# Kernel tuning notes

Hardware: AMD Instinct MI355X
Metric: run time of the kernel (lower is better)

Reference implementation:

```python
import jax, jax.numpy as jnp
import numpy as np

N = 16384; C = 16; H = 256; W = 704
HEADS = 4; PTS = 4; K = 8; DH = C // HEADS
EPS = 1e-3  # BatchNorm eps from module

def _bn(x, g, b):
    # BatchNorm1d in training mode: batch statistics over N
    mu = x.mean(axis=0)
    var = x.var(axis=0)
    return (x - mu) * jax.lax.rsqrt(var + EPS) * g + b

def setup_inputs():
    key = jax.random.key(0)
    ks = jax.random.split(key, 20)
    def w(i, shape, s=0.25):
        return jax.random.normal(ks[i], shape, jnp.float32) * s
    grid_y = jax.random.randint(ks[0], (N,), 0, H)
    grid_x = jax.random.randint(ks[1], (N,), 0, W)
    return {
        "point_features": jax.random.normal(ks[2], (N, C), jnp.float32),
        "image_feat": jax.random.normal(ks[3], (C, H, W), jnp.float32),
        "image_grid": jnp.stack([grid_y, grid_x], axis=1),
        "Wk": w(4, (C, C)), "bk": w(5, (C,)), "gk": jnp.ones((C,)), "betak": jnp.zeros((C,)),
        "Wfc": w(6, (2, C)), "bfc": w(7, (C,)), "gfc": jnp.ones((C,)), "betafc": jnp.zeros((C,)),
        "Wt": w(8, (C, C)), "bt": w(9, (C,)), "gt": jnp.ones((C,)), "betat": jnp.zeros((C,)),
        "Woff": w(10, (C, HEADS * PTS * 2), 0.02), "boff": w(11, (HEADS * PTS * 2,), 0.5),
        "Wattn": w(12, (C, HEADS * PTS), 0.02), "battn": jnp.zeros((HEADS * PTS,)),
        "Wval": w(13, (C, C)), "bval": w(14, (C,)),
        "Wout": w(15, (C, C)), "bout": w(16, (C,)),
        "Wf": w(17, (2 * C, C)), "bf": w(18, (C,)), "gf": jnp.ones((C,)), "betaf": jnp.zeros((C,)),
    }

def _deform_attn(q, image_feat, grid_f, Woff, boff, Wattn, battn, Wval, bval, Wout, bout):
    # MSDeformAttn with 1 level: learned offsets around projected pixel, bilinear sampling
    n = q.shape[0]
    off = (q @ Woff + boff).reshape(n, HEADS, PTS, 2)
    attn = jax.nn.softmax((q @ Wattn + battn).reshape(n, HEADS, PTS), axis=-1)
    val = (image_feat.reshape(C, H * W).T @ Wval + bval).reshape(H * W, HEADS, DH)
    val_h = val.transpose(1, 0, 2)  # [HEADS, HW, DH]
    loc_y = grid_f[:, 0][:, None, None] + off[..., 0]  # [N, HEADS, PTS]
    loc_x = grid_f[:, 1][:, None, None] + off[..., 1]
    y0 = jnp.floor(loc_y); x0 = jnp.floor(loc_x)
    wy = loc_y - y0; wx = loc_x - x0

    def corner(yi, xi, wgt):
        valid = (yi >= 0) & (yi <= H - 1) & (xi >= 0) & (xi <= W - 1)
        yc = jnp.clip(yi, 0, H - 1).astype(jnp.int32)
        xc = jnp.clip(xi, 0, W - 1).astype(jnp.int32)
        idx = (yc * W + xc).transpose(1, 0, 2)  # [HEADS, N, PTS]
        g = jax.vmap(lambda v, i: v[i])(val_h, idx)  # [HEADS, N, PTS, DH]
        return g * (wgt * valid).transpose(1, 0, 2)[..., None]

    samp = (corner(y0, x0, (1 - wy) * (1 - wx))
            + corner(y0, x0 + 1, (1 - wy) * wx)
            + corner(y0 + 1, x0, wy * (1 - wx))
            + corner(y0 + 1, x0 + 1, wy * wx))  # [HEADS, N, PTS, DH]
    out = (samp * attn.transpose(1, 0, 2)[..., None]).sum(axis=2)  # [HEADS, N, DH]
    out = out.transpose(1, 0, 2).reshape(n, C)
    return out @ Wout + bout

def reference(point_features, image_feat, image_grid, Wk, bk, gk, betak, Wfc, bfc, gfc, betafc, Wt, bt, gt, betat, Woff, boff, Wattn, battn, Wval, bval, Wout, bout, Wf, bf, gf, betaf):
    grid_f = image_grid.astype(jnp.float32)
    # KNN over projected pixel coords (cKDTree.query k=K+1, drop self)
    d2 = ((grid_f[:, None, :] - grid_f[None, :, :]) ** 2).sum(-1)
    _, nidx = jax.lax.top_k(-d2, K + 1)
    nidx = nidx[:, 1:]  # [N, K]

    pts = _bn(point_features @ Wk + bk, gk, betak)  # pts_key_proj
    # normalized relative image-plane positions -> fc
    center = grid_f.mean(axis=0)
    rel = grid_f - center
    mx = jnp.abs(rel).max(axis=0)
    mx = jnp.where(mx == 0, 1.0, mx)
    pos = _bn((rel / mx) @ Wfc + bfc, gfc, betafc)

    # gather image feats at projected pixels + KNN-graph neighbor aggregation
    gathered = image_feat[:, image_grid[:, 0], image_grid[:, 1]].T  # [N, C]
    neigh = gathered[nidx].mean(axis=1)  # [N, C]

    q = pts + pos
    img_pre = _deform_attn(q, image_feat, grid_f, Woff, boff, Wattn, battn, Wval, bval, Wout, bout) + neigh

    pts_pre = _bn(pts @ Wt + bt, gt, betat)  # pts_transform
    fuse = jax.nn.relu(jnp.concatenate([pts_pre, img_pre], axis=-1))  # activate_out
    return jax.nn.relu(_bn(fuse @ Wf + bf, gf, betaf))  # fuse_conv
```

## Files before the change

### kernel.cpp

```cpp
#include <hip/hip_runtime.h>
#include <climits>

#define N_ 16384
#define C_ 16
#define H_ 256
#define W_ 704
#define HW_ (H_*W_)
#define NC_ (N_*C_)
#define EPS_ 1e-3f
#define HDR_ 512

typedef unsigned long long ull;


#define VAL_  (HDR_ + 9*NC_)
#define KNNI_ (VAL_ + HW_*16)
#define PARTF_ (KNNI_ + 378256)

__device__ __forceinline__ float wsum64(float v){
#pragma unroll
  for (int o = 32; o > 0; o >>= 1) v += __shfl_down(v, o);
  return v;
}

#define LOAD16(dst, src) { const float4* _s=(const float4*)(src); float4 _a=_s[0],_b=_s[1],_c=_s[2],_d=_s[3]; \
  dst[0]=_a.x;dst[1]=_a.y;dst[2]=_a.z;dst[3]=_a.w; dst[4]=_b.x;dst[5]=_b.y;dst[6]=_b.z;dst[7]=_b.w; \
  dst[8]=_c.x;dst[9]=_c.y;dst[10]=_c.z;dst[11]=_c.w; dst[12]=_d.x;dst[13]=_d.y;dst[14]=_d.z;dst[15]=_d.w; }

#define STORE16(dst, src) { float4* _d=(float4*)(dst); \
  _d[0]=make_float4(src[0],src[1],src[2],src[3]); _d[1]=make_float4(src[4],src[5],src[6],src[7]); \
  _d[2]=make_float4(src[8],src[9],src[10],src[11]); _d[3]=make_float4(src[12],src[13],src[14],src[15]); }

__global__ __launch_bounds__(256) void k_init(float* ws){
  if (blockIdx.x < 176){
    int4* c = (int4*)(ws + KNNI_);
    c[blockIdx.x*256 + threadIdx.x] = make_int4(0,0,0,0);
  } else if (threadIdx.x == 0){
    int* ih = (int*)ws;
    ih[0]=0; ih[1]=0; ih[2]=INT_MAX; ih[3]=INT_MIN; ih[4]=INT_MAX; ih[5]=INT_MIN;
  }
}

__global__ __launch_bounds__(256) void k_gridcnt(const int* __restrict__ grid, float* __restrict__ ws){
  int i = blockIdx.x*256 + threadIdx.x;
  int2 p = ((const int2*)grid)[i];
  int* counts = (int*)(ws + KNNI_);
  atomicAdd(&counts[p.x*W_ + p.y], 1);
  int sy=p.x, sx=p.y, mny=p.x, mxy=p.x, mnx=p.y, mxx=p.y;
#pragma unroll
  for (int o=32;o>0;o>>=1){
    sy += __shfl_down(sy,o); sx += __shfl_down(sx,o);
    mny = min(mny,__shfl_down(mny,o)); mxy = max(mxy,__shfl_down(mxy,o));
    mnx = min(mnx,__shfl_down(mnx,o)); mxx = max(mxx,__shfl_down(mxx,o));
  }
  __shared__ int sh[24];
  int w = threadIdx.x >> 6;
  if ((threadIdx.x & 63) == 0){
    sh[w]=sy; sh[4+w]=sx; sh[8+w]=mny; sh[12+w]=mxy; sh[16+w]=mnx; sh[20+w]=mxx;
  }
  __syncthreads();
  if (threadIdx.x == 0){
    int a0=sh[0]+sh[1]+sh[2]+sh[3];
    int a1=sh[4]+sh[5]+sh[6]+sh[7];
    int a2=min(min(sh[8],sh[9]),min(sh[10],sh[11]));
    int a3=max(max(sh[12],sh[13]),max(sh[14],sh[15]));
    int a4=min(min(sh[16],sh[17]),min(sh[18],sh[19]));
    int a5=max(max(sh[20],sh[21]),max(sh[22],sh[23]));
    int* ih = (int*)ws;
    atomicAdd(&ih[0],a0); atomicAdd(&ih[1],a1);
    atomicMin(&ih[2],a2); atomicMax(&ih[3],a3);
    atomicMin(&ih[4],a4); atomicMax(&ih[5],a5);
  }
}

__global__ __launch_bounds__(256) void k_scanA(float* ws){
  const int* counts = (const int*)(ws + KNNI_);
  int* bsum = (int*)(ws + KNNI_) + 180224 + 180240;
  int t = threadIdx.x;
  int v = counts[blockIdx.x*256 + t];
#pragma unroll
  for (int o=32;o>0;o>>=1) v += __shfl_down(v,o);
  __shared__ int w4[4];
  if ((t&63)==0) w4[t>>6] = v;
  __syncthreads();
  if (t==0) bsum[blockIdx.x] = w4[0]+w4[1]+w4[2]+w4[3];
}

__global__ __launch_bounds__(256) void k_scanB(float* ws){
  if (threadIdx.x == 0){
    int* ih = (int*)ws;
    float cy = (float)ih[0] / (float)N_;
    float cx = (float)ih[1] / (float)N_;
    float my = fmaxf((float)ih[3]-cy, cy-(float)ih[2]);
    float mx = fmaxf((float)ih[5]-cx, cx-(float)ih[4]);
    if (my == 0.f) my = 1.f;
    if (mx == 0.f) mx = 1.f;
    ws[264]=cy; ws[265]=cx; ws[266]=1.f/my; ws[267]=1.f/mx;
  }
  int* bsum = (int*)(ws + KNNI_) + 180224 + 180240;
  int* boff = bsum + 704;
  __shared__ int tmp[256];
  __shared__ int carry;
  int t = threadIdx.x;
  if (t==0) carry = 0;
  __syncthreads();
  for (int c=0;c<3;++c){
    int idx = c*256 + t;
    int v = (idx < 704) ? bsum[idx] : 0;
    tmp[t] = v;
    __syncthreads();
    for (int o=1;o<256;o<<=1){
      int x = (t>=o) ? tmp[t-o] : 0;
      __syncthreads();
      tmp[t] += x;
      __syncthreads();
    }
    int incl = tmp[t];
    int base = carry;
    if (idx < 704) boff[idx] = base + incl - v;
    __syncthreads();
    if (t==255) carry = base + incl;
    __syncthreads();
  }
}

__global__ __launch_bounds__(256) void k_scanC(float* ws){
  int* counts = (int*)(ws + KNNI_);
  int* cellst = counts + 180224;
  const int* boff = counts + 180224 + 180240 + 704;
  __shared__ int tmp[256];
  int t = threadIdx.x;
  int i = blockIdx.x*256 + t;
  int v = counts[i];
  tmp[t] = v;
  __syncthreads();
  for (int o=1;o<256;o<<=1){
    int x = (t>=o) ? tmp[t-o] : 0;
    __syncthreads();
    tmp[t] += x;
    __syncthreads();
  }
  int start = boff[blockIdx.x] + tmp[t] - v;
  cellst[i] = start;
  counts[i] = start;
  if (i == 0) cellst[HW_] = N_;
}

__global__ __launch_bounds__(256) void k_scatter(const int* __restrict__ grid, float* __restrict__ ws){
  int i = blockIdx.x*256 + threadIdx.x;
  int2 g = ((const int2*)grid)[i];
  int* counts = (int*)(ws + KNNI_);
  unsigned* psort = (unsigned*)(counts + 180224 + 180240 + 704 + 704);
  int pos = atomicAdd(&counts[g.x*W_ + g.y], 1);
  psort[pos] = ((unsigned)g.x<<24) | ((unsigned)g.y<<14) | (unsigned)i;
}

__global__ __launch_bounds__(256) void k_gath(const float* __restrict__ imf,
                                              const int* __restrict__ grid,
                                              float* __restrict__ ws){
  int idx = blockIdx.x*256 + threadIdx.x;
  int i = idx >> 4, c = idx & 15;
  int2 g = ((const int2*)grid)[i];
  ws[HDR_ + 2*NC_ + idx] = imf[c*HW_ + g.x*W_ + g.y];
}

__global__ __launch_bounds__(64) void k_knn2(float* __restrict__ ws){
  int gid = blockIdx.x*64 + threadIdx.x;
  const int* cellst = (const int*)(ws + KNNI_) + 180224;
  const unsigned* psort = (const unsigned*)((const int*)(ws + KNNI_) + 180224 + 180240 + 704 + 704);
  unsigned me = psort[gid];
  int y = (int)(me>>24), x = (int)((me>>14)&1023), i = (int)(me&16383);
  int r = 8;
  for (;;){
    int y0=max(y-r,0), y1=min(y+r,H_-1), x0=max(x-r,0), x1=min(x+r,W_-1);
    bool covered = (y0==0)&&(y1==H_-1)&&(x0==0)&&(x1==W_-1);
    int area = (y1-y0+1)*(x1-x0+1);
    if (area >= 224 || covered) break;
    r += 8;
  }
  ull arr[9];
  for (;;){
    int y0=max(y-r,0), y1=min(y+r,H_-1), x0=max(x-r,0), x1=min(x+r,W_-1);
    bool covered = (y0==0)&&(y1==H_-1)&&(x0==0)&&(x1==W_-1);
#pragma unroll
    for (int q=0;q<9;++q) arr[q] = ~0ull;
    for (int yy=y0; yy<=y1; ++yy){
      int rowb = yy*W_;
      int s = cellst[rowb + x0];
      int e = cellst[rowb + x1 + 1];
      for (int p=s; p<e; ++p){
        unsigned u = psort[p];
        int py = (int)(u>>24), px = (int)((u>>14)&1023), pi = (int)(u&16383);
        int dy = y-py, dx = x-px;
        int d2 = dy*dy + dx*dx;
        ull key = ((ull)(unsigned)d2 << 14) | (unsigned)pi;
        if (key < arr[8]){
          int q = 8;
          while (q > 0 && arr[q-1] > key){ arr[q] = arr[q-1]; --q; }
          arr[q] = key;
        }
      }
    }
    if (covered) break;
    if (arr[8] != ~0ull){
      int d9 = (int)(arr[8] >> 14);
      if (d9 < (r+1)*(r+1)) break;
    }
    r <<= 1;
  }
  const float* gath = ws + HDR_ + 2*NC_;
  float acc[16];
#pragma unroll
  for (int c=0;c<16;++c) acc[c] = 0.f;
  for (int nb=1; nb<9; ++nb){
    int idx = (int)(arr[nb] & 16383ull);
    const float4* s4 = (const float4*)(gath + idx*16);
#pragma unroll
    for (int rq=0; rq<4; ++rq){
      float4 v = s4[rq];
      acc[rq*4]+=v.x; acc[rq*4+1]+=v.y; acc[rq*4+2]+=v.z; acc[rq*4+3]+=v.w;
    }
  }
  float* neigh = ws + HDR_ + 7*NC_;
  float o[16];
#pragma unroll
  for (int c=0;c<16;++c) o[c] = acc[c]*0.125f;
  STORE16(neigh + i*16, o);
}

__global__ __launch_bounds__(64) void k_lin1(
    const float* __restrict__ pf, const int* __restrict__ grid,
    const float* __restrict__ Wk, const float* __restrict__ bk,
    const float* __restrict__ Wfc, const float* __restrict__ bfc,
    float* __restrict__ ws)
{
  __shared__ float sWk[256], sbk[16], sWfc[32], sbfc[16];
  int t = threadIdx.x;
  for (int j=t;j<256;j+=64) sWk[j] = Wk[j];
  if (t < 16){ sbk[t]=bk[t]; sbfc[t]=bfc[t]; }
  if (t < 32) sWfc[t] = Wfc[t];
  __syncthreads();
  int i = blockIdx.x*64 + t;
  float p[16]; LOAD16(p, pf + i*16);
  float ok[16];
#pragma unroll
  for (int c=0;c<16;++c) ok[c] = sbk[c];
#pragma unroll
  for (int j=0;j<16;++j){ float v = p[j];
#pragma unroll
    for (int c=0;c<16;++c) ok[c] += v*sWk[j*16+c];
  }
  float* pts_lin = ws + HDR_;
  STORE16(pts_lin + i*16, ok);
  float cy=ws[264], cx=ws[265], imy=ws[266], imx=ws[267];
  int2 g = ((const int2*)grid)[i];
  float ry = ((float)g.x - cy)*imy, rx = ((float)g.y - cx)*imx;
  float op[16];
#pragma unroll
  for (int c=0;c<16;++c) op[c] = ry*sWfc[c] + rx*sWfc[16+c] + sbfc[c];
  float* pos_lin = ws + HDR_ + NC_;
  STORE16(pos_lin + i*16, op);
  float* partK  = ws + VAL_;
  float* partFC = ws + VAL_ + 8192;
#pragma unroll
  for (int c=0;c<16;++c){
    float a = wsum64(ok[c]); float b = wsum64(ok[c]*ok[c]);
    if (t==0){ partK[blockIdx.x*32+c]=a; partK[blockIdx.x*32+16+c]=b; }
    a = wsum64(op[c]); b = wsum64(op[c]*op[c]);
    if (t==0){ partFC[blockIdx.x*32+c]=a; partFC[blockIdx.x*32+16+c]=b; }
  }
}

__device__ __forceinline__ void red1_body(const float* __restrict__ g, const float* __restrict__ b,
                                          float* __restrict__ ws, int partOff, int aOff, float* red){
  int t = threadIdx.x, slot = t & 31, chunk = t >> 5;
  const float* part = ws + partOff;
  float acc = 0.f;
  for (int bb=chunk*32; bb<chunk*32+32; ++bb) acc += part[bb*32 + slot];
  red[t] = acc;
  __syncthreads();
  if (chunk == 0){
    float v = red[slot];
#pragma unroll
    for (int k2=1;k2<8;++k2) v += red[k2*32+slot];
    red[slot] = v;
  }
  __syncthreads();
  if (t < 16){
    float mu  = red[t]    * (1.f/N_);
    float var = red[16+t] * (1.f/N_) - mu*mu;
    float a = g[t] / sqrtf(var + EPS_);
    ws[aOff+t]    = a;
    ws[aOff+16+t] = b[t] - mu*a;
  }
  __syncthreads();
}

__global__ __launch_bounds__(256) void k_red2(const float* __restrict__ gk, const float* __restrict__ betak,
                                              const float* __restrict__ gfc, const float* __restrict__ betafc,
                                              float* __restrict__ ws){
  __shared__ float red[256];
  red1_body(gk, betak, ws, VAL_, 136, red);
  red1_body(gfc, betafc, ws, VAL_+8192, 168, red);
}

__global__ __launch_bounds__(256) void k_red1(const float* __restrict__ g, const float* __restrict__ b,
                                              float* __restrict__ ws, int partOff, int aOff){
  __shared__ float red[256];
  red1_body(g, b, ws, partOff, aOff, red);
}

__global__ __launch_bounds__(64) void k_qstage(
    const float* __restrict__ Wt, const float* __restrict__ bt,
    const float* __restrict__ Woff, const float* __restrict__ boff,
    const float* __restrict__ Wattn, const float* __restrict__ battn,
    float* __restrict__ ws)
{
  __shared__ float sWt[256], sWoff[512], sWattn[256];
  __shared__ float sbt[16], sboff[32], sbattn[16];
  __shared__ float skA[16], skC[16], sfcA[16], sfcC[16];
  int t = threadIdx.x;
  for (int j=t;j<256;j+=64){ sWt[j]=Wt[j]; sWattn[j]=Wattn[j]; }
  for (int j=t;j<512;j+=64) sWoff[j]=Woff[j];
  if (t<16){ sbt[t]=bt[t]; sbattn[t]=battn[t];
    skA[t]=ws[136+t]; skC[t]=ws[152+t]; sfcA[t]=ws[168+t]; sfcC[t]=ws[184+t]; }
  if (t<32) sboff[t]=boff[t];
  __syncthreads();
  int i = blockIdx.x*64 + t;
  float* pts_lin = ws + HDR_;
  float* pos_lin = ws + HDR_ + NC_;
  float* t_lin   = ws + HDR_ + 3*NC_;
  float* offp    = ws + HDR_ + 4*NC_;
  float* attnp   = ws + HDR_ + 6*NC_;
  float pl[16], po[16];
  LOAD16(pl, pts_lin + i*16);
  LOAD16(po, pos_lin + i*16);
  float pts[16], q[16];
#pragma unroll
  for (int c=0;c<16;++c){ pts[c] = pl[c]*skA[c]+skC[c]; q[c] = pts[c] + po[c]*sfcA[c]+sfcC[c]; }
  float tv[16];
#pragma unroll
  for (int c=0;c<16;++c) tv[c] = sbt[c];
#pragma unroll
  for (int j=0;j<16;++j){ float v=pts[j];
#pragma unroll
    for (int c=0;c<16;++c) tv[c] += v*sWt[j*16+c];
  }
  STORE16(t_lin + i*16, tv);
  float* partT = ws + VAL_ + 16384;
#pragma unroll
  for (int c=0;c<16;++c){
    float a = wsum64(tv[c]); float b = wsum64(tv[c]*tv[c]);
    if (t==0){ partT[blockIdx.x*32+c]=a; partT[blockIdx.x*32+16+c]=b; }
  }
  float ov[32];
#pragma unroll
  for (int o=0;o<32;++o) ov[o] = sboff[o];
#pragma unroll
  for (int j=0;j<16;++j){ float v=q[j];
#pragma unroll
    for (int o=0;o<32;++o) ov[o] += v*sWoff[j*32+o];
  }
  { float4* d=(float4*)(offp + i*32);
#pragma unroll
    for (int r=0;r<8;++r) d[r]=make_float4(ov[r*4],ov[r*4+1],ov[r*4+2],ov[r*4+3]);
  }
  float l[16];
#pragma unroll
  for (int c=0;c<16;++c) l[c] = sbattn[c];
#pragma unroll
  for (int j=0;j<16;++j){ float v=q[j];
#pragma unroll
    for (int c=0;c<16;++c) l[c] += v*sWattn[j*16+c];
  }
  float av[16];
#pragma unroll
  for (int h=0;h<4;++h){
    float m = fmaxf(fmaxf(l[h*4],l[h*4+1]),fmaxf(l[h*4+2],l[h*4+3]));
    float e0=expf(l[h*4]-m), e1=expf(l[h*4+1]-m), e2=expf(l[h*4+2]-m), e3=expf(l[h*4+3]-m);
    float inv = 1.f/(e0+e1+e2+e3);
    av[h*4]=e0*inv; av[h*4+1]=e1*inv; av[h*4+2]=e2*inv; av[h*4+3]=e3*inv;
  }
  STORE16(attnp + i*16, av);
}

__global__ __launch_bounds__(256) void k_val(const float* __restrict__ imf,
    const float* __restrict__ Wval, const float* __restrict__ bval, float* __restrict__ ws)
{
  __shared__ float sW[256], sb[16];
  int t = threadIdx.x;
  sW[t] = Wval[t];
  if (t < 16) sb[t] = bval[t];
  __syncthreads();
  int pix = blockIdx.x*256 + t;
  float a[16];
#pragma unroll
  for (int ci=0;ci<16;++ci) a[ci] = imf[ci*HW_ + pix];
  float o[16];
#pragma unroll
  for (int c=0;c<16;++c) o[c] = sb[c];
#pragma unroll
  for (int ci=0;ci<16;++ci){ float v=a[ci];
#pragma unroll
    for (int c=0;c<16;++c) o[c] += v*sW[ci*16+c];
  }
  float* val = ws + VAL_;
  STORE16(val + pix*16, o);
}

__global__ __launch_bounds__(256) void k_attn(
    const int* __restrict__ grid,
    const float* __restrict__ Wout, const float* __restrict__ bout,
    const float* __restrict__ Wf, const float* __restrict__ bf,
    float* __restrict__ ws)
{
  __shared__ float sWout[256], sWf[512], sbout[16], sbf[16];
  __shared__ float sTl[1024], sNei[1024], sSamp[1024], sImg[1024];
  __shared__ float sPart[128];
  int t = threadIdx.x;
  int p = t >> 2, h = t & 3;
  int i = blockIdx.x*64 + p;
  sWout[t]=Wout[t]; sWf[t]=Wf[t]; sWf[t+256]=Wf[t+256];
  if (t<16){ sbout[t]=bout[t]; sbf[t]=bf[t]; }
  {
    const float4* tl4 = (const float4*)(ws + HDR_ + 3*NC_ + blockIdx.x*1024);
    const float4* nv4 = (const float4*)(ws + HDR_ + 7*NC_ + blockIdx.x*1024);
    float4 v = tl4[t];
    int c0 = (t*4) & 15;
    float a0=ws[200+c0],a1=ws[200+c0+1],a2=ws[200+c0+2],a3=ws[200+c0+3];
    float c0v=ws[216+c0],c1v=ws[216+c0+1],c2v=ws[216+c0+2],c3v=ws[216+c0+3];
    sTl[t*4]   = fmaxf(v.x*a0+c0v, 0.f);
    sTl[t*4+1] = fmaxf(v.y*a1+c1v, 0.f);
    sTl[t*4+2] = fmaxf(v.z*a2+c2v, 0.f);
    sTl[t*4+3] = fmaxf(v.w*a3+c3v, 0.f);
    float4 nv = nv4[t];
    sNei[t*4]=nv.x; sNei[t*4+1]=nv.y; sNei[t*4+2]=nv.z; sNei[t*4+3]=nv.w;
  }
  const float4* off4 = (const float4*)(ws + HDR_ + 4*NC_ + blockIdx.x*2048);
  float4 o0 = off4[t*2], o1 = off4[t*2+1];
  float4 aw = ((const float4*)(ws + HDR_ + 6*NC_ + blockIdx.x*1024))[t];
  int2 g = ((const int2*)grid)[i];
  float y = (float)g.x, x = (float)g.y;
  const float4* val4 = (const float4*)(ws + VAL_);
  float4 acc = make_float4(0.f,0.f,0.f,0.f);
  float offv[8] = {o0.x,o0.y,o0.z,o0.w,o1.x,o1.y,o1.z,o1.w};
  float avv[4]  = {aw.x,aw.y,aw.z,aw.w};
#define CORNER(yy,xx,wgt) do{ int _y=(yy),_x=(xx); \
    if ((unsigned)_y < (unsigned)H_ && (unsigned)_x < (unsigned)W_){ \
      float4 _v = val4[(_y*W_+_x)*4 + h]; float _w = a*(wgt); \
      acc.x += _w*_v.x; acc.y += _w*_v.y; acc.z += _w*_v.z; acc.w += _w*_v.w; } }while(0)
#pragma unroll
  for (int pt=0; pt<4; ++pt){
    float a  = avv[pt];
    float ly = y + offv[pt*2], lx = x + offv[pt*2+1];
    float fy = floorf(ly), fx = floorf(lx);
    float wy = ly - fy, wx = lx - fx;
    int y0 = (int)fy, x0 = (int)fx;
    CORNER(y0,   x0,   (1.f-wy)*(1.f-wx));
    CORNER(y0,   x0+1, (1.f-wy)*wx);
    CORNER(y0+1, x0,   wy*(1.f-wx));
    CORNER(y0+1, x0+1, wy*wx);
  }
#undef CORNER
  ((float4*)sSamp)[t] = acc;
  __syncthreads();
  float img[4];
#pragma unroll
  for (int k=0;k<4;++k){ int cc=h*4+k; img[k] = sbout[cc] + sNei[p*16+cc]; }
#pragma unroll
  for (int j=0;j<16;++j){
    float v = sSamp[p*16+j];
#pragma unroll
    for (int k=0;k<4;++k) img[k] += v*sWout[j*16 + h*4 + k];
  }
  ((float4*)sImg)[t] = make_float4(img[0],img[1],img[2],img[3]);
  __syncthreads();
  float fl[4];
#pragma unroll
  for (int k=0;k<4;++k) fl[k] = sbf[h*4+k];
#pragma unroll
  for (int j=0;j<16;++j){
    float v1 = sTl[p*16+j];
    float v2 = fmaxf(sImg[p*16+j], 0.f);
#pragma unroll
    for (int k=0;k<4;++k){
      fl[k] += v1*sWf[j*16 + h*4 + k];
      fl[k] += v2*sWf[(16+j)*16 + h*4 + k];
    }
  }
  float* f_lin = ws + HDR_ + 8*NC_;
  ((float4*)(f_lin + blockIdx.x*1024))[t] = make_float4(fl[0],fl[1],fl[2],fl[3]);
  float s0=fl[0],s1=fl[1],s2=fl[2],s3=fl[3];
  float q0=fl[0]*fl[0],q1=fl[1]*fl[1],q2=fl[2]*fl[2],q3=fl[3]*fl[3];
#pragma unroll
  for (int o=32;o>=4;o>>=1){
    s0+=__shfl_down(s0,o); s1+=__shfl_down(s1,o); s2+=__shfl_down(s2,o); s3+=__shfl_down(s3,o);
    q0+=__shfl_down(q0,o); q1+=__shfl_down(q1,o); q2+=__shfl_down(q2,o); q3+=__shfl_down(q3,o);
  }
  int wave = t >> 6, lane = t & 63;
  if (lane < 4){
    sPart[wave*32 + lane*4+0]=s0; sPart[wave*32 + lane*4+1]=s1;
    sPart[wave*32 + lane*4+2]=s2; sPart[wave*32 + lane*4+3]=s3;
    sPart[wave*32 + 16 + lane*4+0]=q0; sPart[wave*32 + 16 + lane*4+1]=q1;
    sPart[wave*32 + 16 + lane*4+2]=q2; sPart[wave*32 + 16 + lane*4+3]=q3;
  }
  __syncthreads();
  if (t < 32){
    float v = sPart[t]+sPart[32+t]+sPart[64+t]+sPart[96+t];
    (ws + PARTF_)[blockIdx.x*32 + t] = v;
  }
}

__global__ __launch_bounds__(256) void k_out(const float* __restrict__ ws, float* __restrict__ out){
  int idx = blockIdx.x*256 + threadIdx.x;
  int c = idx & 15;
  float v = ws[HDR_ + 8*NC_ + idx];
  out[idx] = fmaxf(v*ws[232+c] + ws[248+c], 0.f);
}

extern "C" void kernel_launch(void* const* d_in, const int* in_sizes, int n_in,
                              void* d_out, int out_size, void* d_ws, size_t ws_size,
                              hipStream_t stream)
{
  const float* pf    = (const float*)d_in[0];
  const float* imf   = (const float*)d_in[1];
  const int*   gridp = (const int*)d_in[2];
  const float* Wk   =(const float*)d_in[3],  *bk   =(const float*)d_in[4];
  const float* gk   =(const float*)d_in[5],  *betak=(const float*)d_in[6];
  const float* Wfc  =(const float*)d_in[7],  *bfc  =(const float*)d_in[8];
  const float* gfc  =(const float*)d_in[9],  *betafc=(const float*)d_in[10];
  const float* Wt   =(const float*)d_in[11], *bt   =(const float*)d_in[12];
  const float* gt   =(const float*)d_in[13], *betat=(const float*)d_in[14];
  const float* Woff =(const float*)d_in[15], *boff =(const float*)d_in[16];
  const float* Wattn=(const float*)d_in[17], *battn=(const float*)d_in[18];
  const float* Wval =(const float*)d_in[19], *bval =(const float*)d_in[20];
  const float* Wout =(const float*)d_in[21], *bout =(const float*)d_in[22];
  const float* Wf   =(const float*)d_in[23], *bf   =(const float*)d_in[24];
  const float* gf   =(const float*)d_in[25], *betaf=(const float*)d_in[26];
  float* ws  = (float*)d_ws;
  float* out = (float*)d_out;

  hipLaunchKernelGGL(k_init,     dim3(177),     dim3(256), 0, stream, ws);
  hipLaunchKernelGGL(k_gridcnt,  dim3(N_/256),  dim3(256), 0, stream, gridp, ws);
  hipLaunchKernelGGL(k_scanA,    dim3(704),     dim3(256), 0, stream, ws);
  hipLaunchKernelGGL(k_scanB,    dim3(1),       dim3(256), 0, stream, ws);
  hipLaunchKernelGGL(k_scanC,    dim3(704),     dim3(256), 0, stream, ws);
  hipLaunchKernelGGL(k_scatter,  dim3(N_/256),  dim3(256), 0, stream, gridp, ws);
  hipLaunchKernelGGL(k_gath,     dim3(NC_/256), dim3(256), 0, stream, imf, gridp, ws);
  hipLaunchKernelGGL(k_lin1,     dim3(N_/64),   dim3(64),  0, stream, pf, gridp, Wk, bk, Wfc, bfc, ws);
  hipLaunchKernelGGL(k_red2,     dim3(1),       dim3(256), 0, stream, gk, betak, gfc, betafc, ws);
  hipLaunchKernelGGL(k_qstage,   dim3(N_/64),   dim3(64),  0, stream, Wt, bt, Woff, boff, Wattn, battn, ws);
  hipLaunchKernelGGL(k_red1,     dim3(1),       dim3(256), 0, stream, gt, betat, ws, VAL_+16384, 200);
  hipLaunchKernelGGL(k_val,      dim3(HW_/256), dim3(256), 0, stream, imf, Wval, bval, ws);
  hipLaunchKernelGGL(k_knn2,     dim3(N_/64),   dim3(64),  0, stream, ws);
  hipLaunchKernelGGL(k_attn,     dim3(N_/64),   dim3(256), 0, stream, gridp, Wout, bout, Wf, bf, ws);
  hipLaunchKernelGGL(k_red1,     dim3(1),       dim3(256), 0, stream, gf, betaf, ws, PARTF_, 232);
  hipLaunchKernelGGL(k_out,      dim3(NC_/256), dim3(256), 0, stream, ws, out);
}
```

Baseline: 275.0 us.

## Parallelize KNN across 4 lanes per point with LDS band cache, fuse gather/val kernels

The KNN kernel now uses four lanes per query point. Each lane scans every fourth row of the search window, and the lanes merge their partial top-9 lists with shuffles. The block first caches the sorted points of its row band in shared memory and binary-searches each row for the x range, falling back to global memory when the band is too large. The gather and value-projection kernels are merged into one launch, and the scan kernels switch from an LDS Hillis-Steele scan to wave shuffle scans. Partial-stat buffers move to new workspace offsets so they no longer alias the value buffer. The costs are extra merge logic, more divergence during expansion rounds, and 24KB of LDS per block.

```diff
diff --git a/kernel.cpp b/kernel.cpp
--- a/kernel.cpp
+++ b/kernel.cpp
@@ -13,9 +13,14 @@
 typedef unsigned long long ull;
 
 
-#define VAL_  (HDR_ + 9*NC_)
-#define KNNI_ (VAL_ + HW_*16)
+#define VAL_   (HDR_ + 9*NC_)
+#define KNNI_  (VAL_ + HW_*16)
 #define PARTF_ (KNNI_ + 378256)
+#define PK_    (PARTF_ + 8192)
+#define PFC_   (PARTF_ + 16384)
+#define PT_    (PARTF_ + 24576)
+
+#define CAP_ 6144
 
 __device__ __forceinline__ float wsum64(float v){
 #pragma unroll
@@ -99,27 +104,24 @@
   }
   int* bsum = (int*)(ws + KNNI_) + 180224 + 180240;
   int* boff = bsum + 704;
-  __shared__ int tmp[256];
-  __shared__ int carry;
-  int t = threadIdx.x;
-  if (t==0) carry = 0;
+  __shared__ int sWsum[4];
+  __shared__ int sCarry;
+  int t = threadIdx.x, lane = t & 63, wv = t >> 6;
+  if (t==0) sCarry = 0;
   __syncthreads();
   for (int c=0;c<3;++c){
     int idx = c*256 + t;
-    int v = (idx < 704) ? bsum[idx] : 0;
-    tmp[t] = v;
+    int v0 = (idx < 704) ? bsum[idx] : 0;
+    int v = v0;
+#pragma unroll
+    for (int o=1;o<64;o<<=1){ int xx=__shfl_up(v,o); if (lane>=o) v+=xx; }
+    if (lane==63) sWsum[wv]=v;
     __syncthreads();
-    for (int o=1;o<256;o<<=1){
-      int x = (t>=o) ? tmp[t-o] : 0;
-      __syncthreads();
-      tmp[t] += x;
-      __syncthreads();
-    }
-    int incl = tmp[t];
-    int base = carry;
-    if (idx < 704) boff[idx] = base + incl - v;
+    int add = sCarry;
+    for (int w2=0;w2<wv;++w2) add += sWsum[w2];
+    if (idx < 704) boff[idx] = add + v - v0;
     __syncthreads();
-    if (t==255) carry = base + incl;
+    if (t==255) sCarry = add + v;
     __syncthreads();
   }
 }
@@ -128,19 +130,17 @@
   int* counts = (int*)(ws + KNNI_);
   int* cellst = counts + 180224;
   const int* boff = counts + 180224 + 180240 + 704;
-  __shared__ int tmp[256];
-  int t = threadIdx.x;
+  __shared__ int sWsum[4];
+  int t = threadIdx.x, lane = t & 63, wv = t >> 6;
   int i = blockIdx.x*256 + t;
-  int v = counts[i];
-  tmp[t] = v;
-  __syncthreads();
-  for (int o=1;o<256;o<<=1){
-    int x = (t>=o) ? tmp[t-o] : 0;
-    __syncthreads();
-    tmp[t] += x;
-    __syncthreads();
-  }
-  int start = boff[blockIdx.x] + tmp[t] - v;
+  int v0 = counts[i], v = v0;
+#pragma unroll
+  for (int o=1;o<64;o<<=1){ int xx=__shfl_up(v,o); if (lane>=o) v+=xx; }
+  if (lane==63) sWsum[wv]=v;
+  __syncthreads();
+  int add = boff[blockIdx.x];
+  for (int w2=0;w2<wv;++w2) add += sWsum[w2];
+  int start = add + v - v0;
   cellst[i] = start;
   counts[i] = start;
   if (i == 0) cellst[HW_] = N_;
@@ -155,77 +155,184 @@
   psort[pos] = ((unsigned)g.x<<24) | ((unsigned)g.y<<14) | (unsigned)i;
 }
 
-__global__ __launch_bounds__(256) void k_gath(const float* __restrict__ imf,
+__global__ __launch_bounds__(256) void k_prep(const float* __restrict__ imf,
                                               const int* __restrict__ grid,
+                                              const float* __restrict__ Wval,
+                                              const float* __restrict__ bval,
                                               float* __restrict__ ws){
-  int idx = blockIdx.x*256 + threadIdx.x;
-  int i = idx >> 4, c = idx & 15;
-  int2 g = ((const int2*)grid)[i];
-  ws[HDR_ + 2*NC_ + idx] = imf[c*HW_ + g.x*W_ + g.y];
-}
-
-__global__ __launch_bounds__(64) void k_knn2(float* __restrict__ ws){
-  int gid = blockIdx.x*64 + threadIdx.x;
+  int t = threadIdx.x;
+  if (blockIdx.x < 1024){
+    int idx = blockIdx.x*256 + t;
+    int i = idx >> 4, c = idx & 15;
+    int2 g = ((const int2*)grid)[i];
+    ws[HDR_ + 2*NC_ + idx] = imf[c*HW_ + g.x*W_ + g.y];
+  } else {
+    __shared__ float sW[256], sb[16];
+    sW[t] = Wval[t];
+    if (t < 16) sb[t] = bval[t];
+    __syncthreads();
+    int pix = (blockIdx.x-1024)*256 + t;
+    float a[16];
+#pragma unroll
+    for (int ci=0;ci<16;++ci) a[ci] = imf[ci*HW_ + pix];
+    float o[16];
+#pragma unroll
+    for (int c=0;c<16;++c) o[c] = sb[c];
+#pragma unroll
+    for (int ci=0;ci<16;++ci){ float v=a[ci];
+#pragma unroll
+      for (int c=0;c<16;++c) o[c] += v*sW[ci*16+c];
+    }
+    float* val = ws + VAL_;
+    STORE16(val + pix*16, o);
+  }
+}
+
+__device__ __forceinline__ void knn_insert(ull* arr, ull key){
+  if (key < arr[8]){
+    int q = 8;
+    while (q > 0 && arr[q-1] > key){ arr[q] = arr[q-1]; --q; }
+    arr[q] = key;
+  }
+}
+
+__device__ __forceinline__ void scan_rows_global(const int* __restrict__ cellst,
+                                                 const unsigned* __restrict__ psort,
+                                                 int y, int x, int s,
+                                                 int y0, int y1, int x0, int x1, ull* arr){
+  for (int yy=y0+s; yy<=y1; yy+=4){
+    int rowb = yy*W_;
+    int st = cellst[rowb + x0];
+    int e  = cellst[rowb + x1 + 1];
+    int dy = y-yy, dy2 = dy*dy;
+    for (int p=st; p<e; ++p){
+      unsigned u = psort[p];
+      int px = (int)((u>>14)&1023);
+      int dx = x-px;
+      knn_insert(arr, ((ull)(unsigned)(dy2+dx*dx) << 14) | (ull)(u & 16383u));
+    }
+  }
+}
+
+__global__ __launch_bounds__(256) void k_knn4(float* __restrict__ ws){
   const int* cellst = (const int*)(ws + KNNI_) + 180224;
   const unsigned* psort = (const unsigned*)((const int*)(ws + KNNI_) + 180224 + 180240 + 704 + 704);
+  __shared__ unsigned sBand[CAP_];
+  __shared__ int sRowBase[80];
+  __shared__ int sMn, sMx;
+  int tid = threadIdx.x, lane = tid & 63;
+  int s = tid & 3, pl = tid >> 2;
+  int gid = blockIdx.x*64 + pl;
   unsigned me = psort[gid];
   int y = (int)(me>>24), x = (int)((me>>14)&1023), i = (int)(me&16383);
+  if (tid==0){ sMn = INT_MAX; sMx = -1; }
+  __syncthreads();
+  if (s==0){ atomicMin(&sMn, y); atomicMax(&sMx, y); }
+  __syncthreads();
+  int ya = max(sMn-16,0), yb = min(sMx+16,H_-1);
+  int nr = yb-ya+1;
+  int p0 = cellst[ya*W_], p1 = cellst[(yb+1)*W_];
+  int count = p1-p0;
+  bool fb = (count > CAP_) || (nr > 78);
+  if (!fb){
+    for (int j=tid; j<count; j+=256) sBand[j] = psort[p0+j];
+    for (int j=tid; j<=nr; j+=256) sRowBase[j] = cellst[(ya+j)*W_] - p0;
+  }
+  __syncthreads();
   int r = 8;
-  for (;;){
-    int y0=max(y-r,0), y1=min(y+r,H_-1), x0=max(x-r,0), x1=min(x+r,W_-1);
-    bool covered = (y0==0)&&(y1==H_-1)&&(x0==0)&&(x1==W_-1);
-    int area = (y1-y0+1)*(x1-x0+1);
-    if (area >= 224 || covered) break;
-    r += 8;
-  }
+  { int y0=max(y-8,0),y1=min(y+8,H_-1),x0=max(x-8,0),x1=min(x+8,W_-1);
+    if ((y1-y0+1)*(x1-x0+1) < 224) r = 16; }
   ull arr[9];
-  for (;;){
-    int y0=max(y-r,0), y1=min(y+r,H_-1), x0=max(x-r,0), x1=min(x+r,W_-1);
-    bool covered = (y0==0)&&(y1==H_-1)&&(x0==0)&&(x1==W_-1);
-#pragma unroll
-    for (int q=0;q<9;++q) arr[q] = ~0ull;
-    for (int yy=y0; yy<=y1; ++yy){
-      int rowb = yy*W_;
-      int s = cellst[rowb + x0];
-      int e = cellst[rowb + x1 + 1];
-      for (int p=s; p<e; ++p){
-        unsigned u = psort[p];
-        int py = (int)(u>>24), px = (int)((u>>14)&1023), pi = (int)(u&16383);
-        int dy = y-py, dx = x-px;
-        int d2 = dy*dy + dx*dx;
-        ull key = ((ull)(unsigned)d2 << 14) | (unsigned)pi;
-        if (key < arr[8]){
-          int q = 8;
-          while (q > 0 && arr[q-1] > key){ arr[q] = arr[q-1]; --q; }
-          arr[q] = key;
+#pragma unroll
+  for (int q=0;q<9;++q) arr[q] = ~0ull;
+  {
+    int y0=max(y-r,0),y1=min(y+r,H_-1),x0=max(x-r,0),x1=min(x+r,W_-1);
+    if (!fb){
+      for (int yy=y0+s; yy<=y1; yy+=4){
+        int j = yy-ya;
+        int b = sRowBase[j], e = sRowBase[j+1];
+        int lo=b, hi=e;
+        while (lo<hi){ int mid=(lo+hi)>>1; int xm=(int)((sBand[mid]>>14)&1023); if (xm<x0) lo=mid+1; else hi=mid; }
+        int dy = y-yy, dy2 = dy*dy;
+        for (int p=lo; p<e; ++p){
+          unsigned u = sBand[p];
+          int px = (int)((u>>14)&1023);
+          if (px > x1) break;
+          int dx = x-px;
+          knn_insert(arr, ((ull)(unsigned)(dy2+dx*dx) << 14) | (ull)(u & 16383u));
         }
       }
-    }
-    if (covered) break;
-    if (arr[8] != ~0ull){
-      int d9 = (int)(arr[8] >> 14);
-      if (d9 < (r+1)*(r+1)) break;
-    }
-    r <<= 1;
+    } else {
+      scan_rows_global(cellst, psort, y, x, s, y0, y1, x0, x1, arr);
+    }
+  }
+  ull m[9];
+  bool done = false;
+  {
+    ull k[9];
+#pragma unroll
+    for (int q=0;q<9;++q) m[q] = ~0ull;
+    int base = lane & ~3;
+    for (int ss=0; ss<4; ++ss){
+#pragma unroll
+      for (int q=0;q<9;++q) k[q] = __shfl(arr[q], base+ss);
+      for (int q2=0;q2<9;++q2){
+        ull kk = k[q2];
+        if (kk >= m[8]) break;
+        int q = 8; while (q>0 && m[q-1]>kk){ m[q]=m[q-1]; --q; } m[q]=kk;
+      }
+    }
+    int y0=max(y-r,0),y1=min(y+r,H_-1),x0=max(x-r,0),x1=min(x+r,W_-1);
+    bool covered = (y0==0)&&(y1==H_-1)&&(x0==0)&&(x1==W_-1);
+    bool ok = covered;
+    if (!ok && m[8] != ~0ull){ int d9 = (int)(m[8]>>14); ok = d9 < (r+1)*(r+1); }
+    done = ok;
+  }
+  while (__ballot(!done)){
+    if (!done){
+      r <<= 1;
+      int y0=max(y-r,0),y1=min(y+r,H_-1),x0=max(x-r,0),x1=min(x+r,W_-1);
+#pragma unroll
+      for (int q=0;q<9;++q) arr[q] = ~0ull;
+      scan_rows_global(cellst, psort, y, x, s, y0, y1, x0, x1, arr);
+    }
+    ull k[9];
+    bool doIns = !done;
+    if (doIns){
+#pragma unroll
+      for (int q=0;q<9;++q) m[q] = ~0ull;
+    }
+    int base = lane & ~3;
+    for (int ss=0; ss<4; ++ss){
+#pragma unroll
+      for (int q=0;q<9;++q) k[q] = __shfl(arr[q], base+ss);
+      if (doIns){
+        for (int q2=0;q2<9;++q2){
+          ull kk = k[q2];
+          if (kk >= m[8]) break;
+          int q = 8; while (q>0 && m[q-1]>kk){ m[q]=m[q-1]; --q; } m[q]=kk;
+        }
+      }
+    }
+    if (!done){
+      int y0=max(y-r,0),y1=min(y+r,H_-1),x0=max(x-r,0),x1=min(x+r,W_-1);
+      bool covered = (y0==0)&&(y1==H_-1)&&(x0==0)&&(x1==W_-1);
+      bool ok = covered;
+      if (!ok && m[8] != ~0ull){ int d9 = (int)(m[8]>>14); ok = d9 < (r+1)*(r+1); }
+      if (ok) done = true;
+    }
   }
   const float* gath = ws + HDR_ + 2*NC_;
-  float acc[16];
-#pragma unroll
-  for (int c=0;c<16;++c) acc[c] = 0.f;
+  float4 acc = make_float4(0.f,0.f,0.f,0.f);
+#pragma unroll
   for (int nb=1; nb<9; ++nb){
-    int idx = (int)(arr[nb] & 16383ull);
-    const float4* s4 = (const float4*)(gath + idx*16);
-#pragma unroll
-    for (int rq=0; rq<4; ++rq){
-      float4 v = s4[rq];
-      acc[rq*4]+=v.x; acc[rq*4+1]+=v.y; acc[rq*4+2]+=v.z; acc[rq*4+3]+=v.w;
-    }
+    int idx = (int)(m[nb] & 16383ull);
+    const float4 g = *(const float4*)(gath + idx*16 + s*4);
+    acc.x += g.x; acc.y += g.y; acc.z += g.z; acc.w += g.w;
   }
   float* neigh = ws + HDR_ + 7*NC_;
-  float o[16];
-#pragma unroll
-  for (int c=0;c<16;++c) o[c] = acc[c]*0.125f;
-  STORE16(neigh + i*16, o);
+  *(float4*)(neigh + i*16 + s*4) =
+      make_float4(acc.x*0.125f, acc.y*0.125f, acc.z*0.125f, acc.w*0.125f);
 }
 
 __global__ __launch_bounds__(64) void k_lin1(
@@ -260,8 +367,8 @@
   for (int c=0;c<16;++c) op[c] = ry*sWfc[c] + rx*sWfc[16+c] + sbfc[c];
   float* pos_lin = ws + HDR_ + NC_;
   STORE16(pos_lin + i*16, op);
-  float* partK  = ws + VAL_;
-  float* partFC = ws + VAL_ + 8192;
+  float* partK  = ws + PK_;
+  float* partFC = ws + PFC_;
 #pragma unroll
   for (int c=0;c<16;++c){
     float a = wsum64(ok[c]); float b = wsum64(ok[c]*ok[c]);
@@ -300,8 +407,8 @@
                                               const float* __restrict__ gfc, const float* __restrict__ betafc,
                                               float* __restrict__ ws){
   __shared__ float red[256];
-  red1_body(gk, betak, ws, VAL_, 136, red);
-  red1_body(gfc, betafc, ws, VAL_+8192, 168, red);
+  red1_body(gk, betak, ws, PK_, 136, red);
+  red1_body(gfc, betafc, ws, PFC_, 168, red);
 }
 
 __global__ __launch_bounds__(256) void k_red1(const float* __restrict__ g, const float* __restrict__ b,
@@ -347,7 +454,7 @@
     for (int c=0;c<16;++c) tv[c] += v*sWt[j*16+c];
   }
   STORE16(t_lin + i*16, tv);
-  float* partT = ws + VAL_ + 16384;
+  float* partT = ws + PT_;
 #pragma unroll
   for (int c=0;c<16;++c){
     float a = wsum64(tv[c]); float b = wsum64(tv[c]*tv[c]);
@@ -382,30 +489,6 @@
     av[h*4]=e0*inv; av[h*4+1]=e1*inv; av[h*4+2]=e2*inv; av[h*4+3]=e3*inv;
   }
   STORE16(attnp + i*16, av);
-}
-
-__global__ __launch_bounds__(256) void k_val(const float* __restrict__ imf,
-    const float* __restrict__ Wval, const float* __restrict__ bval, float* __restrict__ ws)
-{
-  __shared__ float sW[256], sb[16];
-  int t = threadIdx.x;
-  sW[t] = Wval[t];
-  if (t < 16) sb[t] = bval[t];
-  __syncthreads();
-  int pix = blockIdx.x*256 + t;
-  float a[16];
-#pragma unroll
-  for (int ci=0;ci<16;++ci) a[ci] = imf[ci*HW_ + pix];
-  float o[16];
-#pragma unroll
-  for (int c=0;c<16;++c) o[c] = sb[c];
-#pragma unroll
-  for (int ci=0;ci<16;++ci){ float v=a[ci];
-#pragma unroll
-    for (int c=0;c<16;++c) o[c] += v*sW[ci*16+c];
-  }
-  float* val = ws + VAL_;
-  STORE16(val + pix*16, o);
 }
 
 __global__ __launch_bounds__(256) void k_attn(
@@ -540,20 +623,19 @@
   float* ws  = (float*)d_ws;
   float* out = (float*)d_out;
 
-  hipLaunchKernelGGL(k_init,     dim3(177),     dim3(256), 0, stream, ws);
-  hipLaunchKernelGGL(k_gridcnt,  dim3(N_/256),  dim3(256), 0, stream, gridp, ws);
-  hipLaunchKernelGGL(k_scanA,    dim3(704),     dim3(256), 0, stream, ws);
-  hipLaunchKernelGGL(k_scanB,    dim3(1),       dim3(256), 0, stream, ws);
-  hipLaunchKernelGGL(k_scanC,    dim3(704),     dim3(256), 0, stream, ws);
-  hipLaunchKernelGGL(k_scatter,  dim3(N_/256),  dim3(256), 0, stream, gridp, ws);
-  hipLaunchKernelGGL(k_gath,     dim3(NC_/256), dim3(256), 0, stream, imf, gridp, ws);
-  hipLaunchKernelGGL(k_lin1,     dim3(N_/64),   dim3(64),  0, stream, pf, gridp, Wk, bk, Wfc, bfc, ws);
-  hipLaunchKernelGGL(k_red2,     dim3(1),       dim3(256), 0, stream, gk, betak, gfc, betafc, ws);
-  hipLaunchKernelGGL(k_qstage,   dim3(N_/64),   dim3(64),  0, stream, Wt, bt, Woff, boff, Wattn, battn, ws);
-  hipLaunchKernelGGL(k_red1,     dim3(1),       dim3(256), 0, stream, gt, betat, ws, VAL_+16384, 200);
-  hipLaunchKernelGGL(k_val,      dim3(HW_/256), dim3(256), 0, stream, imf, Wval, bval, ws);
-  hipLaunchKernelGGL(k_knn2,     dim3(N_/64),   dim3(64),  0, stream, ws);
-  hipLaunchKernelGGL(k_attn,     dim3(N_/64),   dim3(256), 0, stream, gridp, Wout, bout, Wf, bf, ws);
-  hipLaunchKernelGGL(k_red1,     dim3(1),       dim3(256), 0, stream, gf, betaf, ws, PARTF_, 232);
-  hipLaunchKernelGGL(k_out,      dim3(NC_/256), dim3(256), 0, stream, ws, out);
-}
+  hipLaunchKernelGGL(k_init,     dim3(177),      dim3(256), 0, stream, ws);
+  hipLaunchKernelGGL(k_gridcnt,  dim3(N_/256),   dim3(256), 0, stream, gridp, ws);
+  hipLaunchKernelGGL(k_scanA,    dim3(704),      dim3(256), 0, stream, ws);
+  hipLaunchKernelGGL(k_scanB,    dim3(1),        dim3(256), 0, stream, ws);
+  hipLaunchKernelGGL(k_scanC,    dim3(704),      dim3(256), 0, stream, ws);
+  hipLaunchKernelGGL(k_scatter,  dim3(N_/256),   dim3(256), 0, stream, gridp, ws);
+  hipLaunchKernelGGL(k_prep,     dim3(1728),     dim3(256), 0, stream, imf, gridp, Wval, bval, ws);
+  hipLaunchKernelGGL(k_lin1,     dim3(N_/64),    dim3(64),  0, stream, pf, gridp, Wk, bk, Wfc, bfc, ws);
+  hipLaunchKernelGGL(k_red2,     dim3(1),        dim3(256), 0, stream, gk, betak, gfc, betafc, ws);
+  hipLaunchKernelGGL(k_qstage,   dim3(N_/64),    dim3(64),  0, stream, Wt, bt, Woff, boff, Wattn, battn, ws);
+  hipLaunchKernelGGL(k_red1,     dim3(1),        dim3(256), 0, stream, gt, betat, ws, PT_, 200);
+  hipLaunchKernelGGL(k_knn4,     dim3(N_/64),    dim3(256), 0, stream, ws);
+  hipLaunchKernelGGL(k_attn,     dim3(N_/64),    dim3(256), 0, stream, gridp, Wout, bout, Wf, bf, ws);
+  hipLaunchKernelGGL(k_red1,     dim3(1),        dim3(256), 0, stream, gf, betaf, ws, PARTF_, 232);
+  hipLaunchKernelGGL(k_out,      dim3(NC_/256),  dim3(256), 0, stream, ws, out);
+}
```

New measurement: 223.0 us. 18.9% less time.
